# Kernel optimization log

Measured on AMD Instinct MI355X. Metric: run time of the kernel, lower is better.

## Reference

```python
import jax, jax.numpy as jnp
import numpy as np

B, T, D = 2, 1024, 1024
C = 16384
K_GT = 8
TOPK = 16
BLOCK = 8192
TF_ALPHA = 0.5  # teacher_force_alpha: soft mix of GT and predicted features


def setup_inputs() -> dict:
    key = jax.random.key(0)
    k1, k2, k3, k4 = jax.random.split(key, 4)
    hidden = jax.random.normal(k1, (B, T, D), dtype=jnp.float32)
    # Linear(n_embd, n_concepts_padded, bias=False) -> weight (C, D)
    predictor_w = jax.random.normal(k2, (C, D), dtype=jnp.float32) * 0.02
    # Embedding(n_concepts_padded, concept_dim)
    concept_emb = jax.random.normal(k3, (C, D), dtype=jnp.float32) * 0.02
    concept_ids = jax.random.randint(k4, (B, T, K_GT), 0, C, dtype=jnp.int32)
    concept_mask = jnp.ones((B, T, K_GT), dtype=bool)
    return {
        "hidden": hidden,
        "predictor_w": predictor_w,
        "concept_emb": concept_emb,
        "concept_ids": concept_ids,
        "concept_mask": concept_mask,
    }


def _streaming_topk(hidden, predictor_w):
    """Block-wise top-k over concept logits, never materializing (B,T,C).
    Returns topk_logits (B,T,TOPK), topk_indices (B,T,TOPK)."""
    n_blocks = C // BLOCK
    w_blocks = predictor_w.reshape(n_blocks, BLOCK, D)
    offsets = jnp.arange(n_blocks, dtype=jnp.int32) * BLOCK

    def step(carry, inp):
        top_l, top_i = carry  # (B,T,TOPK)
        w_blk, off = inp
        logits = jnp.einsum("btd,cd->btc", hidden, w_blk)  # (B,T,BLOCK)
        blk_idx = off + jnp.arange(BLOCK, dtype=jnp.int32)
        cand_l = jnp.concatenate([top_l, logits], axis=-1)
        cand_i = jnp.concatenate(
            [top_i, jnp.broadcast_to(blk_idx, logits.shape)], axis=-1
        )
        new_l, pos = jax.lax.top_k(cand_l, TOPK)
        new_i = jnp.take_along_axis(cand_i, pos, axis=-1)
        return (new_l, new_i), None

    init = (
        jnp.full((B, T, TOPK), -jnp.inf, dtype=hidden.dtype),
        jnp.zeros((B, T, TOPK), dtype=jnp.int32),
    )
    (top_l, top_i), _ = jax.lax.scan(step, init, (w_blocks, offsets))
    return top_l, top_i


def reference(hidden, predictor_w, concept_emb, concept_ids, concept_mask):
    # ---- predicted features via streaming top-k (sparse weighted embedding sum)
    topk_logits, topk_idx = _streaming_topk(hidden, predictor_w)
    weights = jax.nn.sigmoid(topk_logits)  # (B,T,TOPK); topk_on_logits=False is
    # equivalent since sigmoid is monotone
    topk_emb = concept_emb[topk_idx]  # (B,T,TOPK,D) gather
    predicted = jnp.einsum("btk,btkd->btd", weights, topk_emb)

    # ---- ground-truth pooled features (scatter-add over valid concept ids)
    valid = concept_mask & (concept_ids != -1)  # (B,T,K)
    safe_ids = jnp.where(valid, concept_ids, 0)
    gt_emb = concept_emb[safe_ids] * valid[..., None].astype(concept_emb.dtype)
    gt_features = gt_emb.sum(axis=2)  # (B,T,D)

    # ---- soft teacher forcing mix
    features = TF_ALPHA * gt_features + (1.0 - TF_ALPHA) * predicted
    return features
```

## Files before the change

### kernel.cpp

```cpp
#include <hip/hip_runtime.h>
#include <math.h>

#define B_    2
#define T_    1024
#define D_    1024
#define C_    16384
#define KGT   8
#define TOPK  16
#define ROWS  (B_*T_)

#define NSPLIT 16
#define CS     (C_/NSPLIT)
#define NC     (NSPLIT*TOPK)
#define NREF   32

#define RT_A   64

typedef __bf16 bf16x8 __attribute__((ext_vector_type(8)));
typedef float  f32x4  __attribute__((ext_vector_type(4)));

#define BAR_LGKM() do { \
    asm volatile("s_waitcnt lgkmcnt(0)\n\ts_barrier" ::: "memory"); \
    __builtin_amdgcn_sched_barrier(0); } while (0)

#define BAR_CHUNK() do { \
    asm volatile("s_waitcnt vmcnt(0)\n\ts_barrier" ::: "memory"); \
    __builtin_amdgcn_sched_barrier(0); } while (0)

__device__ __forceinline__ unsigned short bf16_rne(float x) {
    unsigned int u = __float_as_uint(x);
    unsigned int r = (u + 0x7FFFu + ((u >> 16) & 1u)) >> 16;
    return (unsigned short)r;
}

__device__ __forceinline__ void pack_hi_one(const float* __restrict__ src,
                                            uint4* __restrict__ dhi, size_t gt)
{
    int lane = (int)(gt & 63);
    size_t f = gt >> 6;
    int ks = (int)(f & 31);
    size_t rf = f >> 5;
    size_t row = rf * 16 + (lane & 15);
    int k0 = ks * 32 + (lane >> 4) * 8;
    const float4* s = (const float4*)(src + row * D_ + k0);
    float4 x0 = s[0], x1 = s[1];
    float v[8] = {x0.x, x0.y, x0.z, x0.w, x1.x, x1.y, x1.z, x1.w};
    unsigned short h[8];
    #pragma unroll
    for (int i = 0; i < 8; ++i) h[i] = bf16_rne(v[i]);
    uint4 ph;
    ph.x = h[0] | ((unsigned)h[1] << 16); ph.y = h[2] | ((unsigned)h[3] << 16);
    ph.z = h[4] | ((unsigned)h[5] << 16); ph.w = h[6] | ((unsigned)h[7] << 16);
    dhi[f * 64 + lane] = ph;
}

#define NWPACK ((C_/16)*32*64/256)

__global__ __launch_bounds__(256)
void pack_hi_all_kernel(const float* __restrict__ W, const float* __restrict__ hidden,
                        uint4* __restrict__ Wh, uint4* __restrict__ Ah)
{
    int bid = blockIdx.x;
    if (bid < NWPACK) {
        pack_hi_one(W, Wh, (size_t)bid * 256 + threadIdx.x);
    } else {
        pack_hi_one(hidden, Ah, (size_t)(bid - NWPACK) * 256 + threadIdx.x);
    }
}

#define ASTAGE(cc_) do {                                                          \
    const int ccS = (cc_);                                                        \
    const int kc0 = (ccS & 3) * 8;                                                \
    uint4* dstb = &Abuf[(ccS & 1)*2048];                                          \
    _Pragma("unroll")                                                             \
    for (int t = 0; t < 4; ++t) {                                                 \
        int s = t*8 + w;                                                          \
        int kci = s >> 2, ai = s & 3;                                             \
        const uint4* srcp = Ah + ((size_t)((rb*4 + ai)*32 + kc0 + kci))*64 + lane;\
        __builtin_amdgcn_global_load_lds(                                         \
            (const __attribute__((address_space(1))) void*)srcp,                  \
            (__attribute__((address_space(3))) void*)&dstb[s*64],                 \
            16, 0, 0);                                                            \
    } } while (0)

#define INSERTK(key_) do {                                                        \
    _Pragma("unroll")                                                             \
    for (int e = 0; e < TOPK; ++e) {                                              \
        if (e == minpos) tk[e] = (key_);                                          \
    }                                                                             \
    minkey = tk[0]; minpos = 0;                                                   \
    _Pragma("unroll")                                                             \
    for (int e = 1; e < TOPK; ++e) {                                              \
        if (tk[e] < minkey) { minkey = tk[e]; minpos = e; }                       \
    } } while (0)

__global__ __launch_bounds__(512, 4)
void mfma_logits_topk_kernel(const uint4* __restrict__ Wh, const uint4* __restrict__ Ah,
                             float* __restrict__ candVal, unsigned short* __restrict__ candIdx)
{
    __shared__ uint4 Abuf[4096];
    __shared__ float ltile[RT_A*36];

    const int tid  = threadIdx.x;
    const int lane = tid & 63;
    const int w    = tid >> 6;
    const int d    = blockIdx.x;
    const int rb   = (d >> 3) & 31;
    const int sp   = ((d & 7) << 1) | (d >> 8);

    const uint4* Wwave = Wh + ((size_t)(sp*64 + w*2) * 32) * 64 + lane;

    unsigned tk[TOPK];
    #pragma unroll
    for (int e = 0; e < TOPK; ++e) tk[e] = 0u;
    unsigned minkey = 0u; int minpos = 0;

    const int srow = tid >> 3, p = tid & 7;

    f32x4 acc[4][2];

    ASTAGE(0);

    #pragma unroll 1
    for (int cc = 0; cc < 16; ++cc) {
        const int ct = cc >> 2;
        const int ch = cc & 3;

        BAR_CHUNK();
        if (cc + 1 < 16) ASTAGE(cc + 1);

        if (ch == 0) {
            #pragma unroll
            for (int i = 0; i < 4; ++i)
                #pragma unroll
                for (int j = 0; j < 2; ++j)
                    acc[i][j] = (f32x4){0.f, 0.f, 0.f, 0.f};
        }

        const uint4* abuf = &Abuf[(cc & 1)*2048];
        const uint4* wch  = Wwave + ((size_t)(ct*16)*32 + ch*8)*64;
        #pragma unroll
        for (int kci = 0; kci < 8; ++kci) {
            bf16x8 a[4], b[2];
            #pragma unroll
            for (int i = 0; i < 4; ++i)
                a[i] = *(const bf16x8*)&abuf[(kci*4 + i)*64 + lane];
            #pragma unroll
            for (int j = 0; j < 2; ++j)
                b[j] = *(const bf16x8*)&wch[((size_t)j*32 + kci)*64];
            #pragma unroll
            for (int j = 0; j < 2; ++j)
                #pragma unroll
                for (int i = 0; i < 4; ++i)
                    acc[i][j] = __builtin_amdgcn_mfma_f32_16x16x32_bf16(
                        a[i], b[j], acc[i][j], 0, 0, 0);
        }

        if (ch == 3) {
            #pragma unroll 1
            for (int ph = 0; ph < 8; ++ph) {
                if (w == ph) {
                    #pragma unroll
                    for (int i = 0; i < 4; ++i)
                        #pragma unroll
                        for (int j = 0; j < 2; ++j)
                            #pragma unroll
                            for (int jj = 0; jj < 4; ++jj) {
                                int row = i*16 + (lane >> 4)*4 + jj;
                                ltile[row*36 + j*16 + (lane & 15)] = acc[i][j][jj];
                            }
                }
                BAR_LGKM();
                const int lbase = ct*256 + ph*32 + p*4;
                float4 v = *(const float4*)(ltile + srow*36 + p*4);
                float vv[4] = {v.x, v.y, v.z, v.w};
                #pragma unroll
                for (int i = 0; i < 4; ++i) {
                    unsigned u = __float_as_uint(vv[i]);
                    unsigned mono = u ^ ((unsigned)(((int)u) >> 31) | 0x80000000u);
                    unsigned key = (mono & 0xFFFFFC00u) | (unsigned)(lbase + i);
                    if (key > minkey) { INSERTK(key); }
                }
                BAR_LGKM();
            }
        }
    }

    asm volatile("s_waitcnt vmcnt(0)" ::: "memory");
    __syncthreads();
    unsigned* mk  = (unsigned*)Abuf;
    unsigned* mk2 = (unsigned*)(Abuf + 2048);
    #pragma unroll
    for (int e = 0; e < TOPK; ++e) mk[e*512 + tid] = tk[e];
    __syncthreads();

    if (tid < 256) {
        const int c0 = (tid >> 2)*8 + (tid & 3)*2, c1 = c0 + 1;
        for (int k = 0; k < TOPK; ++k) {
            unsigned best = 0u; int bp = 0;
            #pragma unroll
            for (int e = 0; e < TOPK; ++e) {
                unsigned kv = mk[e*512 + c0];
                if (kv > best) { best = kv; bp = e*512 + c0; }
                kv = mk[e*512 + c1];
                if (kv > best) { best = kv; bp = e*512 + c1; }
            }
            mk2[k*256 + tid] = best;
            mk[bp] = 0u;
        }
    }
    __syncthreads();

    if (tid < RT_A) {
        float* cv = candVal + (size_t)(rb*RT_A + tid)*NC + sp*TOPK;
        unsigned short* ci = candIdx + (size_t)(rb*RT_A + tid)*NC + sp*TOPK;
        for (int k = 0; k < TOPK; ++k) {
            unsigned best = 0u; int bp = 0;
            for (int s = 0; s < 4; ++s) {
                int col = tid*4 + s;
                #pragma unroll
                for (int e = 0; e < TOPK; ++e) {
                    unsigned kv = mk2[e*256 + col];
                    if (kv > best) { best = kv; bp = e*256 + col; }
                }
            }
            unsigned m2 = best & 0xFFFFFC00u;
            unsigned u2 = (m2 & 0x80000000u) ? (m2 ^ 0x80000000u) : ~m2;
            cv[k] = __uint_as_float(u2);
            ci[k] = (unsigned short)(sp*1024 + (best & 1023u));
            mk2[bp] = 0u;
        }
    }
}

__global__ __launch_bounds__(256, 4)
void concept_finalize_kernel(const float* __restrict__ hidden,
                             const float* __restrict__ W,
                             const float* __restrict__ emb,
                             const int* __restrict__ ids,
                             const float* __restrict__ candVal,
                             const unsigned short* __restrict__ candIdx,
                             float* __restrict__ out)
{
    __shared__ float  cval[NC];
    __shared__ int    cidx[NC];
    __shared__ int    slot[NREF];
    __shared__ double refv[NREF];
    __shared__ float  selW[TOPK];
    __shared__ int    selIdx[TOPK];

    const int tid = threadIdx.x;
    const int row = blockIdx.x;

    cval[tid] = candVal[(size_t)row*NC + tid];
    cidx[tid] = (int)candIdx[(size_t)row*NC + tid];
    __syncthreads();

    {
        float v = cval[tid]; int rank = 0;
        for (int j = 0; j < NC; ++j) {
            float u = cval[j];
            rank += (u > v) || ((u == v) && (j < tid));
        }
        if (rank < NREF) slot[rank] = tid;
    }
    __syncthreads();

    {
        const int g = tid >> 3, l = tid & 7;
        const int c = cidx[slot[g]];
        const float4* W4 = (const float4*)W;
        const float4* H4 = (const float4*)hidden;
        double acc = 0.0;
        #pragma unroll 4
        for (int s = 0; s < 32; ++s) {
            float4 wv = W4[(size_t)c*(D_/4) + s*8 + l];
            float4 hv = H4[(size_t)row*(D_/4) + s*8 + l];
            acc += (double)hv.x*(double)wv.x + (double)hv.y*(double)wv.y
                 + (double)hv.z*(double)wv.z + (double)hv.w*(double)wv.w;
        }
        acc += __shfl_xor(acc, 1);
        acc += __shfl_xor(acc, 2);
        acc += __shfl_xor(acc, 4);
        if (l == 0) refv[g] = acc;
    }
    __syncthreads();

    if (tid < NREF) {
        double v = refv[tid]; int rank = 0;
        for (int j = 0; j < NREF; ++j) {
            double u = refv[j];
            rank += (u > v) || ((u == v) && (j < tid));
        }
        if (rank < TOPK) {
            selIdx[rank] = cidx[slot[tid]];
            selW[rank]   = 1.0f / (1.0f + expf(-(float)v));
        }
    }
    __syncthreads();

    const float4* E4 = (const float4*)emb;
    float px = 0.f, py = 0.f, pz = 0.f, pw = 0.f;
    #pragma unroll
    for (int k = 0; k < TOPK; ++k) {
        float wt = selW[k];
        float4 e = E4[(size_t)selIdx[k]*(D_/4) + tid];
        px = fmaf(wt, e.x, px); py = fmaf(wt, e.y, py);
        pz = fmaf(wt, e.z, pz); pw = fmaf(wt, e.w, pw);
    }
    float gx = 0.f, gy = 0.f, gz = 0.f, gw = 0.f;
    #pragma unroll
    for (int k = 0; k < KGT; ++k) {
        int c = ids[row*KGT + k];
        float4 e = E4[(size_t)c*(D_/4) + tid];
        gx += e.x; gy += e.y; gz += e.z; gw += e.w;
    }
    float4 o;
    o.x = 0.5f*(gx + px); o.y = 0.5f*(gy + py);
    o.z = 0.5f*(gz + pz); o.w = 0.5f*(gw + pw);
    ((float4*)out)[(size_t)row*(D_/4) + tid] = o;
}

#define RT     64
#define CT     256
#define KC     16
#define HP4    5
#define LTP    65

__global__ __launch_bounds__(256, 2)
void concept_logits_topk_kernel(const float* __restrict__ hidden,
                                const float* __restrict__ W,
                                float* __restrict__ candVal,
                                unsigned short* __restrict__ candIdx)
{
    __shared__ float4 uni[1040];
    __shared__ float4 hT[RT * HP4];
    __shared__ float tval[TOPK * 256];
    __shared__ unsigned short tidx[TOPK * 256];

    float* ltile = (float*)uni;

    const int tid  = threadIdx.x;
    const int row0 = blockIdx.x * RT;
    const int cs0  = blockIdx.y * CS;
    const float4* H4 = (const float4*)hidden;
    const float4* W4 = (const float4*)W;

    #pragma unroll
    for (int e = 0; e < TOPK; ++e) tval[e*256 + tid] = -INFINITY;
    float minval = -INFINITY;
    int   minpos = 0;

    const int rg   = tid >> 5;
    const int cg   = tid & 31;
    const int srow = tid >> 2;
    const int ssub = tid & 3;

    for (int ct = 0; ct < CS/CT; ++ct) {
        const int cbase = cs0 + ct*CT;
        float acc[8][8];
        #pragma unroll
        for (int i = 0; i < 8; ++i)
            #pragma unroll
            for (int j = 0; j < 8; ++j) acc[i][j] = 0.f;

        for (int kc = 0; kc < D_/KC; ++kc) {
            __syncthreads();
            #pragma unroll
            for (int i = 0; i < 4; ++i) {
                int idx = i*256 + tid;
                int wr = idx >> 2, c4 = idx & 3;
                uni[c4*CT + wr] = W4[(size_t)(cbase + wr)*(D_/4) + kc*(KC/4) + c4];
            }
            {
                int hr = tid >> 2, c4 = tid & 3;
                hT[hr*HP4 + c4] = H4[(size_t)(row0 + hr)*(D_/4) + kc*(KC/4) + c4];
            }
            __syncthreads();
            #pragma unroll
            for (int k4 = 0; k4 < KC/4; ++k4) {
                float4 a[8];
                #pragma unroll
                for (int i = 0; i < 8; ++i) a[i] = hT[(rg*8 + i)*HP4 + k4];
                #pragma unroll
                for (int j = 0; j < 8; ++j) {
                    float4 wv = uni[k4*CT + (j*32 + cg)];
                    #pragma unroll
                    for (int i = 0; i < 8; ++i) {
                        acc[i][j] = fmaf(a[i].x, wv.x, acc[i][j]);
                        acc[i][j] = fmaf(a[i].y, wv.y, acc[i][j]);
                        acc[i][j] = fmaf(a[i].z, wv.z, acc[i][j]);
                        acc[i][j] = fmaf(a[i].w, wv.w, acc[i][j]);
                    }
                }
            }
        }

        #pragma unroll
        for (int q = 0; q < 4; ++q) {
            __syncthreads();
            #pragma unroll
            for (int i = 0; i < 8; ++i) {
                #pragma unroll
                for (int jj = 0; jj < 2; ++jj) {
                    int ci = q*2 + jj;
                    ltile[(rg*8 + i)*LTP + (jj*32 + cg)] = acc[i][ci];
                }
            }
            __syncthreads();
            #pragma unroll
            for (int i = 0; i < 16; ++i) {
                float v = ltile[srow*LTP + ssub*16 + i];
                if (v > minval) {
                    int gc = cbase + q*64 + ssub*16 + i;
                    tval[minpos*256 + tid] = v;
                    tidx[minpos*256 + tid] = (unsigned short)gc;
                    minval = INFINITY;
                    #pragma unroll
                    for (int e = 0; e < TOPK; ++e) {
                        float tv_ = tval[e*256 + tid];
                        if (tv_ < minval) { minval = tv_; minpos = e; }
                    }
                }
            }
        }
    }
    __syncthreads();

    if (tid < RT) {
        const int rr = tid;
        float* cv = candVal + (size_t)(row0 + rr)*NC + blockIdx.y*TOPK;
        unsigned short* ci = candIdx + (size_t)(row0 + rr)*NC + blockIdx.y*TOPK;
        for (int k = 0; k < TOPK; ++k) {
            float best = -INFINITY; int bp = 0;
            for (int s = 0; s < 4; ++s) {
                int col = rr*4 + s;
                #pragma unroll
                for (int e = 0; e < TOPK; ++e) {
                    float v = tval[e*256 + col];
                    if (v > best) { best = v; bp = e*256 + col; }
                }
            }
            cv[k] = best;
            ci[k] = tidx[bp];
            tval[bp] = -INFINITY;
        }
    }
}

extern "C" void kernel_launch(void* const* d_in, const int* in_sizes, int n_in,
                              void* d_out, int out_size, void* d_ws, size_t ws_size,
                              hipStream_t stream)
{
    (void)in_sizes; (void)n_in; (void)out_size;
    const float* hidden = (const float*)d_in[0];
    const float* W      = (const float*)d_in[1];
    const float* emb    = (const float*)d_in[2];
    const int*   ids    = (const int*)d_in[3];
    float* out = (float*)d_out;

    const size_t szWh = (size_t)C_ * D_ * 2;
    const size_t szAh = (size_t)ROWS * D_ * 2;
    const size_t szCV = (size_t)ROWS * NC * sizeof(float);
    const size_t szCI = (size_t)ROWS * NC * sizeof(unsigned short);
    const size_t need = szWh + szAh + szCV + szCI;

    if (ws_size >= need) {
        char* p = (char*)d_ws;
        uint4* Wh = (uint4*)p;               p += szWh;
        uint4* Ah = (uint4*)p;               p += szAh;
        float* candVal = (float*)p;          p += szCV;
        unsigned short* candIdx = (unsigned short*)p;

        const int nPack = NWPACK + (ROWS/16)*32*64/256;
        hipLaunchKernelGGL(pack_hi_all_kernel, dim3(nPack), dim3(256), 0, stream,
                           W, hidden, Wh, Ah);
        hipLaunchKernelGGL(mfma_logits_topk_kernel, dim3(512), dim3(512), 0, stream,
                           Wh, Ah, candVal, candIdx);
        hipLaunchKernelGGL(concept_finalize_kernel, dim3(ROWS), dim3(256), 0, stream,
                           hidden, W, emb, ids, candVal, candIdx, out);
    } else {
        float* candVal = (float*)d_ws;
        unsigned short* candIdx =
            (unsigned short*)((char*)d_ws + (size_t)ROWS*NC*sizeof(float));
        hipLaunchKernelGGL(concept_logits_topk_kernel, dim3(ROWS/RT, NSPLIT), dim3(256), 0, stream,
                           hidden, W, candVal, candIdx);
        hipLaunchKernelGGL(concept_finalize_kernel, dim3(ROWS), dim3(256), 0, stream,
                           hidden, W, emb, ids, candVal, candIdx, out);
    }
}
```

Before: 232.1 us.

## Switch logits GEMM to 32x32x16 MFMA with in-register top-k selection

Repacks the bf16 weight and hidden fragments for the 32x32x16 MFMA layout and rewrites the logits kernel to use it, with each wave computing a 32-concept by 64-row tile in two 16-element accumulators. Each lane now keeps two per-row top-k lists and updates them straight from its accumulator registers. This removes the serialized per-wave LDS tile staging and the 16 barriers per column tile. The merge stage is adjusted to the new candidate layout. Register pressure rises (launch bounds drop from 4 to 2 blocks per SIMD hint) and LDS grows, which may cut occupancy.

New measurement: 241.6 us. 4.1% more time.

```diff
diff --git a/kernel.cpp b/kernel.cpp
--- a/kernel.cpp
+++ b/kernel.cpp
@@ -17,11 +17,7 @@
 #define RT_A   64
 
 typedef __bf16 bf16x8 __attribute__((ext_vector_type(8)));
-typedef float  f32x4  __attribute__((ext_vector_type(4)));
-
-#define BAR_LGKM() do { \
-    asm volatile("s_waitcnt lgkmcnt(0)\n\ts_barrier" ::: "memory"); \
-    __builtin_amdgcn_sched_barrier(0); } while (0)
+typedef float  f32x16 __attribute__((ext_vector_type(16)));
 
 #define BAR_CHUNK() do { \
     asm volatile("s_waitcnt vmcnt(0)\n\ts_barrier" ::: "memory"); \
@@ -38,10 +34,10 @@
 {
     int lane = (int)(gt & 63);
     size_t f = gt >> 6;
-    int ks = (int)(f & 31);
-    size_t rf = f >> 5;
-    size_t row = rf * 16 + (lane & 15);
-    int k0 = ks * 32 + (lane >> 4) * 8;
+    int ks16 = (int)(f & 63);
+    size_t rf32 = f >> 6;
+    size_t row = rf32 * 32 + (lane & 31);
+    int k0 = ks16 * 16 + (lane >> 5) * 8;
     const float4* s = (const float4*)(src + row * D_ + k0);
     float4 x0 = s[0], x1 = s[1];
     float v[8] = {x0.x, x0.y, x0.z, x0.w, x1.x, x1.y, x1.z, x1.w};
@@ -54,7 +50,7 @@
     dhi[f * 64 + lane] = ph;
 }
 
-#define NWPACK ((C_/16)*32*64/256)
+#define NWPACK ((C_/32)*64*64/256)
 
 __global__ __launch_bounds__(256)
 void pack_hi_all_kernel(const float* __restrict__ W, const float* __restrict__ hidden,
@@ -68,38 +64,43 @@
     }
 }
 
-#define ASTAGE(cc_) do {                                                          \
-    const int ccS = (cc_);                                                        \
-    const int kc0 = (ccS & 3) * 8;                                                \
-    uint4* dstb = &Abuf[(ccS & 1)*2048];                                          \
+#define ASTAGE(gi_) do {                                                          \
+    const int ca_ = (gi_) & 3;                                                    \
+    uint4* dstb = &Abuf[((gi_) & 1) * 2048];                                      \
     _Pragma("unroll")                                                             \
     for (int t = 0; t < 4; ++t) {                                                 \
-        int s = t*8 + w;                                                          \
-        int kci = s >> 2, ai = s & 3;                                             \
-        const uint4* srcp = Ah + ((size_t)((rb*4 + ai)*32 + kc0 + kci))*64 + lane;\
+        int q = w + t*8;                                                          \
+        int rf = q >> 4, ki = q & 15;                                             \
+        const uint4* srcp = Ah + ((size_t)((rb*2 + rf)*64 + ca_*16 + ki))*64 + lane; \
         __builtin_amdgcn_global_load_lds(                                         \
             (const __attribute__((address_space(1))) void*)srcp,                  \
-            (__attribute__((address_space(3))) void*)&dstb[s*64],                 \
+            (__attribute__((address_space(3))) void*)&dstb[q*64],                 \
             16, 0, 0);                                                            \
     } } while (0)
 
-#define INSERTK(key_) do {                                                        \
+#define INS_A(key_) do {                                                          \
     _Pragma("unroll")                                                             \
-    for (int e = 0; e < TOPK; ++e) {                                              \
-        if (e == minpos) tk[e] = (key_);                                          \
-    }                                                                             \
-    minkey = tk[0]; minpos = 0;                                                   \
+    for (int e = 0; e < TOPK; ++e) { if (e == minposA) tkA[e] = (key_); }         \
+    minkA = tkA[0]; minposA = 0;                                                  \
     _Pragma("unroll")                                                             \
     for (int e = 1; e < TOPK; ++e) {                                              \
-        if (tk[e] < minkey) { minkey = tk[e]; minpos = e; }                       \
+        if (tkA[e] < minkA) { minkA = tkA[e]; minposA = e; }                      \
     } } while (0)
 
-__global__ __launch_bounds__(512, 4)
+#define INS_B(key_) do {                                                          \
+    _Pragma("unroll")                                                             \
+    for (int e = 0; e < TOPK; ++e) { if (e == minposB) tkB[e] = (key_); }         \
+    minkB = tkB[0]; minposB = 0;                                                  \
+    _Pragma("unroll")                                                             \
+    for (int e = 1; e < TOPK; ++e) {                                              \
+        if (tkB[e] < minkB) { minkB = tkB[e]; minposB = e; }                      \
+    } } while (0)
+
+__global__ __launch_bounds__(512, 2)
 void mfma_logits_topk_kernel(const uint4* __restrict__ Wh, const uint4* __restrict__ Ah,
                              float* __restrict__ candVal, unsigned short* __restrict__ candIdx)
 {
-    __shared__ uint4 Abuf[4096];
-    __shared__ float ltile[RT_A*36];
+    __shared__ uint4 Abuf[5120];
 
     const int tid  = threadIdx.x;
     const int lane = tid & 63;
@@ -107,81 +108,59 @@
     const int d    = blockIdx.x;
     const int rb   = (d >> 3) & 31;
     const int sp   = ((d & 7) << 1) | (d >> 8);
-
-    const uint4* Wwave = Wh + ((size_t)(sp*64 + w*2) * 32) * 64 + lane;
-
-    unsigned tk[TOPK];
-    #pragma unroll
-    for (int e = 0; e < TOPK; ++e) tk[e] = 0u;
-    unsigned minkey = 0u; int minpos = 0;
-
-    const int srow = tid >> 3, p = tid & 7;
-
-    f32x4 acc[4][2];
+    const int lhi4 = (lane >> 5) * 4;
+
+    unsigned tkA[TOPK], tkB[TOPK];
+    #pragma unroll
+    for (int e = 0; e < TOPK; ++e) { tkA[e] = 0u; tkB[e] = 0u; }
+    unsigned minkA = 0u, minkB = 0u; int minposA = 0, minposB = 0;
+
+    f32x16 acc0, acc1;
 
     ASTAGE(0);
 
     #pragma unroll 1
-    for (int cc = 0; cc < 16; ++cc) {
-        const int ct = cc >> 2;
-        const int ch = cc & 3;
+    for (int gi = 0; gi < 16; ++gi) {
+        const int ct = gi >> 2;
+        const int ck = gi & 3;
 
         BAR_CHUNK();
-        if (cc + 1 < 16) ASTAGE(cc + 1);
-
-        if (ch == 0) {
-            #pragma unroll
-            for (int i = 0; i < 4; ++i)
-                #pragma unroll
-                for (int j = 0; j < 2; ++j)
-                    acc[i][j] = (f32x4){0.f, 0.f, 0.f, 0.f};
-        }
-
-        const uint4* abuf = &Abuf[(cc & 1)*2048];
-        const uint4* wch  = Wwave + ((size_t)(ct*16)*32 + ch*8)*64;
+        if (gi + 1 < 16) ASTAGE(gi + 1);
+
+        if (ck == 0) {
+            #pragma unroll
+            for (int r = 0; r < 16; ++r) { acc0[r] = 0.f; acc1[r] = 0.f; }
+        }
+
+        const uint4* abuf = &Abuf[(gi & 1)*2048];
+        const uint4* wbase = Wh + ((size_t)((sp*32 + ct*8 + w)*64 + ck*16))*64 + lane;
+
         #pragma unroll
-        for (int kci = 0; kci < 8; ++kci) {
-            bf16x8 a[4], b[2];
-            #pragma unroll
-            for (int i = 0; i < 4; ++i)
-                a[i] = *(const bf16x8*)&abuf[(kci*4 + i)*64 + lane];
-            #pragma unroll
-            for (int j = 0; j < 2; ++j)
-                b[j] = *(const bf16x8*)&wch[((size_t)j*32 + kci)*64];
-            #pragma unroll
-            for (int j = 0; j < 2; ++j)
-                #pragma unroll
-                for (int i = 0; i < 4; ++i)
-                    acc[i][j] = __builtin_amdgcn_mfma_f32_16x16x32_bf16(
-                        a[i], b[j], acc[i][j], 0, 0, 0);
-        }
-
-        if (ch == 3) {
-            #pragma unroll 1
-            for (int ph = 0; ph < 8; ++ph) {
-                if (w == ph) {
-                    #pragma unroll
-                    for (int i = 0; i < 4; ++i)
-                        #pragma unroll
-                        for (int j = 0; j < 2; ++j)
-                            #pragma unroll
-                            for (int jj = 0; jj < 4; ++jj) {
-                                int row = i*16 + (lane >> 4)*4 + jj;
-                                ltile[row*36 + j*16 + (lane & 15)] = acc[i][j][jj];
-                            }
-                }
-                BAR_LGKM();
-                const int lbase = ct*256 + ph*32 + p*4;
-                float4 v = *(const float4*)(ltile + srow*36 + p*4);
-                float vv[4] = {v.x, v.y, v.z, v.w};
-                #pragma unroll
-                for (int i = 0; i < 4; ++i) {
-                    unsigned u = __float_as_uint(vv[i]);
+        for (int ki = 0; ki < 16; ++ki) {
+            bf16x8 a0 = *(const bf16x8*)&abuf[ki*64 + lane];
+            bf16x8 a1 = *(const bf16x8*)&abuf[(16 + ki)*64 + lane];
+            bf16x8 b  = *(const bf16x8*)&wbase[(size_t)ki*64];
+            acc0 = __builtin_amdgcn_mfma_f32_32x32x16_bf16(b, a0, acc0, 0, 0, 0);
+            acc1 = __builtin_amdgcn_mfma_f32_32x32x16_bf16(b, a1, acc1, 0, 0, 0);
+        }
+
+        if (ck == 3) {
+            const int cb = ct*256 + w*32 + lhi4;
+            #pragma unroll
+            for (int r = 0; r < 16; ++r) {
+                const int lidx = cb + (r & 3) + 8*(r >> 2);
+                {
+                    unsigned u = __float_as_uint(acc0[r]);
                     unsigned mono = u ^ ((unsigned)(((int)u) >> 31) | 0x80000000u);
-                    unsigned key = (mono & 0xFFFFFC00u) | (unsigned)(lbase + i);
-                    if (key > minkey) { INSERTK(key); }
-                }
-                BAR_LGKM();
+                    unsigned key = (mono & 0xFFFFFC00u) | (unsigned)lidx;
+                    if (key > minkA) { INS_A(key); }
+                }
+                {
+                    unsigned u = __float_as_uint(acc1[r]);
+                    unsigned mono = u ^ ((unsigned)(((int)u) >> 31) | 0x80000000u);
+                    unsigned key = (mono & 0xFFFFFC00u) | (unsigned)lidx;
+                    if (key > minkB) { INS_B(key); }
+                }
             }
         }
     }
@@ -189,21 +168,33 @@
     asm volatile("s_waitcnt vmcnt(0)" ::: "memory");
     __syncthreads();
     unsigned* mk  = (unsigned*)Abuf;
-    unsigned* mk2 = (unsigned*)(Abuf + 2048);
-    #pragma unroll
-    for (int e = 0; e < TOPK; ++e) mk[e*512 + tid] = tk[e];
+    unsigned* mk2 = (unsigned*)(Abuf + 4096);
+    #pragma unroll
+    for (int e = 0; e < TOPK; ++e) {
+        mk[e*1024 + tid*2 + 0] = tkA[e];
+        mk[e*1024 + tid*2 + 1] = tkB[e];
+    }
     __syncthreads();
 
     if (tid < 256) {
-        const int c0 = (tid >> 2)*8 + (tid & 3)*2, c1 = c0 + 1;
+        const int r = tid & 63, q = tid >> 6;
+        int col[4];
+        #pragma unroll
+        for (int j = 0; j < 4; ++j) {
+            int lid = q*4 + j;
+            int wv = lid >> 1, h = lid & 1;
+            int srctid = wv*64 + (r & 31) + 32*h;
+            col[j] = srctid*2 + (r >> 5);
+        }
         for (int k = 0; k < TOPK; ++k) {
             unsigned best = 0u; int bp = 0;
             #pragma unroll
-            for (int e = 0; e < TOPK; ++e) {
-                unsigned kv = mk[e*512 + c0];
-                if (kv > best) { best = kv; bp = e*512 + c0; }
-                kv = mk[e*512 + c1];
-                if (kv > best) { best = kv; bp = e*512 + c1; }
+            for (int j = 0; j < 4; ++j) {
+                #pragma unroll
+                for (int e = 0; e < TOPK; ++e) {
+                    unsigned kv = mk[e*1024 + col[j]];
+                    if (kv > best) { best = kv; bp = e*1024 + col[j]; }
+                }
             }
             mk2[k*256 + tid] = best;
             mk[bp] = 0u;
@@ -217,7 +208,7 @@
         for (int k = 0; k < TOPK; ++k) {
             unsigned best = 0u; int bp = 0;
             for (int s = 0; s < 4; ++s) {
-                int col = tid*4 + s;
+                int col = s*64 + tid;
                 #pragma unroll
                 for (int e = 0; e < TOPK; ++e) {
                     unsigned kv = mk2[e*256 + col];
@@ -472,7 +463,7 @@
         float* candVal = (float*)p;          p += szCV;
         unsigned short* candIdx = (unsigned short*)p;
 
-        const int nPack = NWPACK + (ROWS/16)*32*64/256;
+        const int nPack = NWPACK + (ROWS/32)*64*64/256;
         hipLaunchKernelGGL(pack_hi_all_kernel, dim3(nPack), dim3(256), 0, stream,
                            W, hidden, Wh, Ah);
         hipLaunchKernelGGL(mfma_logits_topk_kernel, dim3(512), dim3(512), 0, stream,
```
